# Kernel tuning notes

Measured on AMD Instinct MI355X. Metric: run time of the kernel, lower is better.

The kernel has to match this reference:

```python
import jax, jax.numpy as jnp
import numpy as np

E, C, H, W = 64, 8, 32, 32  # E zonotope rows (1 center + 63 error terms)


def setup_inputs() -> dict:
    key = jax.random.key(0)
    x = jax.random.normal(key, (E, C, H, W), dtype=jnp.float32)
    # Zero center => lower < 0 < upper everywhere, so every element crosses
    # and the number of new error terms equals C*H*W (fixed output shape).
    x = x.at[0].set(0.0)
    return {"x": x}


def reference(x):
    e = x.shape[0]
    content_shape = x.shape[1:]
    n = int(np.prod(content_shape))  # max possible new error terms

    err = jnp.sum(jnp.abs(x[1:]), axis=0)
    upper = x[0] + err
    lower = x[0] - err

    cross = (lower * upper < 0).astype(x.dtype)   # crossing-zero mask
    nonneg = (lower >= 0).astype(x.dtype)         # strictly positive mask

    lam = nonneg + cross * upper / (upper - lower)
    lam = jnp.where(jnp.isnan(lam), 0.5, lam)
    # torch assigns lambda via .data (detached from the autograd graph)
    lam = jax.lax.stop_gradient(lam)

    delta = jnp.maximum(-lam * lower, (1.0 - lam) * upper)

    head = (delta / 2 + lam * x[0]) * cross + x[0] * nonneg          # new center
    body = x[1:] * (lam * cross + nonneg)                            # scaled old error terms

    # Vectorized stream-compaction scatter replacing the scripted .item() loop:
    # element k (flat order) with cross==True goes to tail row cumsum(cross)[k]-1.
    flat_cond = cross.reshape(-1) > 0
    vals = (delta / 2).reshape(-1)
    rows = jnp.cumsum(flat_cond.astype(jnp.int32)) - 1
    rows = jnp.clip(rows, 0, n - 1)
    tail = jnp.zeros((n, n), dtype=x.dtype)
    # (row, col) pairs are unique per column; masked-out elements write 0 (no-op).
    tail = tail.at[rows, jnp.arange(n)].set(jnp.where(flat_cond, vals, 0.0))

    return jnp.concatenate(
        [head[None], body, tail.reshape((n,) + content_shape)], axis=0
    )
```

## Files before the change

### kernel.cpp

```cpp
#include <hip/hip_runtime.h>
#include <math.h>

#define EROWS 64
#define NCOL  8192
#define TAIL_OFF (EROWS * NCOL)
#define ROW_F4  (NCOL / 4)
#define BODY_F4 ((EROWS - 1) * ROW_F4)
#define BODY_BLOCKS (BODY_F4 / 256)
#define TAIL_BLOCKS NCOL

typedef float vf4 __attribute__((ext_vector_type(4)));
typedef int   vi4 __attribute__((ext_vector_type(4)));

#define WS_VAL(ws)     ((float*)(ws))
#define WS_FLAG(ws)    ((int*)((char*)(ws) + 32768))
#define WS_COLOF(ws)   ((int*)((char*)(ws) + 65536))
#define WS_TAILVAL(ws) ((float*)((char*)(ws) + 98304))
#define WS_COUNT(ws)   ((int*)((char*)(ws) + 131072))
#define WS_SCALE(ws)   ((float*)((char*)(ws) + 135168))

__global__ void colstats_kernel(const float* __restrict__ x,
                                float* __restrict__ out,
                                float* __restrict__ val,
                                int* __restrict__ flag,
                                float* __restrict__ scale) {
    int k = blockIdx.x * blockDim.x + threadIdx.x;
    if (k >= NCOL) return;

    float err = 0.f;
    for (int e = 1; e < EROWS; ++e)
        err += fabsf(x[e * NCOL + k]);

    float x0    = x[k];
    float upper = x0 + err;
    float lower = x0 - err;

    float cross  = (lower * upper < 0.f) ? 1.f : 0.f;
    float nonneg = (lower >= 0.f) ? 1.f : 0.f;

    float lam = nonneg + cross * upper / (upper - lower);
    if (isnan(lam)) lam = 0.5f;

    float delta = fmaxf(-lam * lower, (1.f - lam) * upper);

    out[k]   = (delta * 0.5f + lam * x0) * cross + x0 * nonneg;
    val[k]   = delta * 0.5f;
    flag[k]  = (cross > 0.f) ? 1 : 0;
    scale[k] = lam * cross + nonneg;
}

__global__ void scan_kernel(const float* __restrict__ val,
                            const int* __restrict__ flag,
                            int* __restrict__ colof,
                            float* __restrict__ tailval,
                            int* __restrict__ count) {
    const int t    = threadIdx.x;
    const int lane = t & 63;
    const int wave = t >> 6;
    const int PER  = NCOL / 256;

    int f[PER];
    int mysum = 0;
    const vi4* fp = (const vi4*)(flag + t * PER);
    for (int j = 0; j < PER / 4; ++j) {
        vi4 v = fp[j];
        f[4*j+0] = v.x; f[4*j+1] = v.y; f[4*j+2] = v.z; f[4*j+3] = v.w;
        mysum += v.x + v.y + v.z + v.w;
    }

    int s = mysum;
    for (int off = 1; off < 64; off <<= 1) {
        int v = __shfl_up(s, off);
        if (lane >= off) s += v;
    }

    __shared__ int wsum[4];
    if (lane == 63) wsum[wave] = s;
    __syncthreads();
    int wbase = 0;
    for (int w = 0; w < wave; ++w) wbase += wsum[w];

    int running = wbase + s - mysum;

    for (int j = 0; j < PER; ++j) {
        int k = t * PER + j;
        if (f[j]) {
            colof[running]   = k;
            tailval[running] = val[k];
            ++running;
        }
    }
    if (t == 255) *count = wsum[0] + wsum[1] + wsum[2] + wsum[3];
}

__global__ void write_kernel(const float* __restrict__ x,
                             const float* __restrict__ scale,
                             const int* __restrict__ colof,
                             const float* __restrict__ tailval,
                             const int* __restrict__ count,
                             float* __restrict__ out) {
    const int tid = threadIdx.x;

    if (blockIdx.x < BODY_BLOCKS) {
        int b = blockIdx.x * 256 + tid;
        int j = b & (ROW_F4 - 1);
        int e = 1 + (b >> 11);
        vf4 xv = ((const vf4*)x)[e * ROW_F4 + j];
        vf4 sv = ((const vf4*)scale)[j];
        ((vf4*)out)[e * ROW_F4 + j] = xv * sv;
    } else {
        int r   = blockIdx.x - BODY_BLOCKS;
        int cnt = *count;
        int   col = (r < cnt) ? colof[r]   : -1;
        float tv  = (r < cnt) ? tailval[r] : 0.f;

        vf4* rowp = (vf4*)out + (TAIL_OFF / 4) + (size_t)r * ROW_F4;
        #pragma unroll
        for (int i = 0; i < ROW_F4 / 256; ++i) {
            int j  = i * 256 + tid;
            int c0 = j << 2;
            vf4 v;
            v.x = (col == c0 + 0) ? tv : 0.f;
            v.y = (col == c0 + 1) ? tv : 0.f;
            v.z = (col == c0 + 2) ? tv : 0.f;
            v.w = (col == c0 + 3) ? tv : 0.f;
            __builtin_nontemporal_store(v, rowp + j);
        }
    }
}

extern "C" void kernel_launch(void* const* d_in, const int* in_sizes, int n_in,
                              void* d_out, int out_size, void* d_ws, size_t ws_size,
                              hipStream_t stream) {
    const float* x = (const float*)d_in[0];
    float* out = (float*)d_out;

    colstats_kernel<<<NCOL / 256, 256, 0, stream>>>(x, out, WS_VAL(d_ws),
                                                    WS_FLAG(d_ws), WS_SCALE(d_ws));
    scan_kernel<<<1, 256, 0, stream>>>(WS_VAL(d_ws), WS_FLAG(d_ws),
                                       WS_COLOF(d_ws), WS_TAILVAL(d_ws), WS_COUNT(d_ws));
    write_kernel<<<BODY_BLOCKS + TAIL_BLOCKS, 256, 0, stream>>>(
        x, WS_SCALE(d_ws), WS_COLOF(d_ws), WS_TAILVAL(d_ws), WS_COUNT(d_ws), out);
}
```

Baseline: 291.2 us.

## Fuse stats with body write and tail zero-fill; scatter diagonal afterwards

Merges column statistics, body scaling and the bulk zero-fill of the tail matrix into one kernel so the large fill does not wait for the scan. A small kernel then writes only the nonzero tail entries after the scan. This removes the per-element compare for the tail and the scale buffer round trip. The fill now uses regular stores instead of nontemporal stores, which may affect cache behaviour.

```diff
diff --git a/kernel.cpp b/kernel.cpp
--- a/kernel.cpp
+++ b/kernel.cpp
@@ -4,10 +4,11 @@
 #define EROWS 64
 #define NCOL  8192
 #define TAIL_OFF (EROWS * NCOL)
-#define ROW_F4  (NCOL / 4)
-#define BODY_F4 ((EROWS - 1) * ROW_F4)
-#define BODY_BLOCKS (BODY_F4 / 256)
-#define TAIL_BLOCKS NCOL
+#define TAIL_F4  (NCOL * NCOL / 4)
+
+#define STAT_BLOCKS 256
+#define FILL_F4_PER_BLOCK 4096
+#define FILL_BLOCKS (TAIL_F4 / FILL_F4_PER_BLOCK)
 
 typedef float vf4 __attribute__((ext_vector_type(4)));
 typedef int   vi4 __attribute__((ext_vector_type(4)));
@@ -17,36 +18,77 @@
 #define WS_COLOF(ws)   ((int*)((char*)(ws) + 65536))
 #define WS_TAILVAL(ws) ((float*)((char*)(ws) + 98304))
 #define WS_COUNT(ws)   ((int*)((char*)(ws) + 131072))
-#define WS_SCALE(ws)   ((float*)((char*)(ws) + 135168))
 
-__global__ void colstats_kernel(const float* __restrict__ x,
-                                float* __restrict__ out,
-                                float* __restrict__ val,
-                                int* __restrict__ flag,
-                                float* __restrict__ scale) {
-    int k = blockIdx.x * blockDim.x + threadIdx.x;
-    if (k >= NCOL) return;
+__global__ void fused_kernel(const float* __restrict__ x,
+                             float* __restrict__ out,
+                             float* __restrict__ val,
+                             int* __restrict__ flag) {
+    const int tid = threadIdx.x;
 
-    float err = 0.f;
-    for (int e = 1; e < EROWS; ++e)
-        err += fabsf(x[e * NCOL + k]);
+    if (blockIdx.x >= STAT_BLOCKS) {
+        vf4 z; z.x = 0.f; z.y = 0.f; z.z = 0.f; z.w = 0.f;
+        vf4* base = (vf4*)out + (TAIL_OFF / 4)
+                  + (size_t)(blockIdx.x - STAT_BLOCKS) * FILL_F4_PER_BLOCK;
+        #pragma unroll
+        for (int i = 0; i < 16; ++i)
+            base[i * 256 + tid] = z;
+        return;
+    }
 
-    float x0    = x[k];
-    float upper = x0 + err;
-    float lower = x0 - err;
+    __shared__ float part[256];
+    __shared__ float sc[32];
 
-    float cross  = (lower * upper < 0.f) ? 1.f : 0.f;
-    float nonneg = (lower >= 0.f) ? 1.f : 0.f;
+    const int c   = tid & 31;
+    const int eg  = tid >> 5;
+    const int col = blockIdx.x * 32 + c;
 
-    float lam = nonneg + cross * upper / (upper - lower);
-    if (isnan(lam)) lam = 0.5f;
+    float xv[8];
+    int   ev[8];
+    int   n = 0;
+    float s = 0.f;
+    #pragma unroll
+    for (int j = 0; j < 8; ++j) {
+        int e = eg + 8 * j;
+        if (e == 0) continue;
+        float v = x[e * NCOL + col];
+        xv[n] = v; ev[n] = e; ++n;
+        s += fabsf(v);
+    }
+    part[eg * 32 + c] = s;
+    __syncthreads();
 
-    float delta = fmaxf(-lam * lower, (1.f - lam) * upper);
+    if (tid < 32) {
+        float err = 0.f;
+        #pragma unroll
+        for (int g = 0; g < 8; ++g)
+            err += part[g * 32 + tid];
 
-    out[k]   = (delta * 0.5f + lam * x0) * cross + x0 * nonneg;
-    val[k]   = delta * 0.5f;
-    flag[k]  = (cross > 0.f) ? 1 : 0;
-    scale[k] = lam * cross + nonneg;
+        int   k  = blockIdx.x * 32 + tid;
+        float x0 = x[k];
+        float upper = x0 + err;
+        float lower = x0 - err;
+
+        float cross  = (lower * upper < 0.f) ? 1.f : 0.f;
+        float nonneg = (lower >= 0.f) ? 1.f : 0.f;
+
+        float lam = nonneg + cross * upper / (upper - lower);
+        if (isnan(lam)) lam = 0.5f;
+
+        float delta = fmaxf(-lam * lower, (1.f - lam) * upper);
+
+        out[k]   = (delta * 0.5f + lam * x0) * cross + x0 * nonneg;
+        val[k]   = delta * 0.5f;
+        flag[k]  = (cross > 0.f) ? 1 : 0;
+        sc[tid]  = lam * cross + nonneg;
+    }
+    __syncthreads();
+
+    float scl = sc[c];
+    #pragma unroll
+    for (int i = 0; i < 8; ++i) {
+        if (i < n)
+            out[ev[i] * NCOL + col] = xv[i] * scl;
+    }
 }
 
 __global__ void scan_kernel(const float* __restrict__ val,
@@ -93,40 +135,14 @@
     if (t == 255) *count = wsum[0] + wsum[1] + wsum[2] + wsum[3];
 }
 
-__global__ void write_kernel(const float* __restrict__ x,
-                             const float* __restrict__ scale,
-                             const int* __restrict__ colof,
-                             const float* __restrict__ tailval,
-                             const int* __restrict__ count,
-                             float* __restrict__ out) {
-    const int tid = threadIdx.x;
-
-    if (blockIdx.x < BODY_BLOCKS) {
-        int b = blockIdx.x * 256 + tid;
-        int j = b & (ROW_F4 - 1);
-        int e = 1 + (b >> 11);
-        vf4 xv = ((const vf4*)x)[e * ROW_F4 + j];
-        vf4 sv = ((const vf4*)scale)[j];
-        ((vf4*)out)[e * ROW_F4 + j] = xv * sv;
-    } else {
-        int r   = blockIdx.x - BODY_BLOCKS;
-        int cnt = *count;
-        int   col = (r < cnt) ? colof[r]   : -1;
-        float tv  = (r < cnt) ? tailval[r] : 0.f;
-
-        vf4* rowp = (vf4*)out + (TAIL_OFF / 4) + (size_t)r * ROW_F4;
-        #pragma unroll
-        for (int i = 0; i < ROW_F4 / 256; ++i) {
-            int j  = i * 256 + tid;
-            int c0 = j << 2;
-            vf4 v;
-            v.x = (col == c0 + 0) ? tv : 0.f;
-            v.y = (col == c0 + 1) ? tv : 0.f;
-            v.z = (col == c0 + 2) ? tv : 0.f;
-            v.w = (col == c0 + 3) ? tv : 0.f;
-            __builtin_nontemporal_store(v, rowp + j);
-        }
-    }
+__global__ void diag_kernel(const int* __restrict__ colof,
+                            const float* __restrict__ tailval,
+                            const int* __restrict__ count,
+                            float* __restrict__ out) {
+    int r = blockIdx.x * blockDim.x + threadIdx.x;
+    int cnt = *count;
+    if (r < cnt)
+        out[TAIL_OFF + (size_t)r * NCOL + colof[r]] = tailval[r];
 }
 
 extern "C" void kernel_launch(void* const* d_in, const int* in_sizes, int n_in,
@@ -135,10 +151,10 @@
     const float* x = (const float*)d_in[0];
     float* out = (float*)d_out;
 
-    colstats_kernel<<<NCOL / 256, 256, 0, stream>>>(x, out, WS_VAL(d_ws),
-                                                    WS_FLAG(d_ws), WS_SCALE(d_ws));
+    fused_kernel<<<STAT_BLOCKS + FILL_BLOCKS, 256, 0, stream>>>(
+        x, out, WS_VAL(d_ws), WS_FLAG(d_ws));
     scan_kernel<<<1, 256, 0, stream>>>(WS_VAL(d_ws), WS_FLAG(d_ws),
                                        WS_COLOF(d_ws), WS_TAILVAL(d_ws), WS_COUNT(d_ws));
-    write_kernel<<<BODY_BLOCKS + TAIL_BLOCKS, 256, 0, stream>>>(
-        x, WS_SCALE(d_ws), WS_COLOF(d_ws), WS_TAILVAL(d_ws), WS_COUNT(d_ws), out);
+    diag_kernel<<<NCOL / 256, 256, 0, stream>>>(WS_COLOF(d_ws), WS_TAILVAL(d_ws),
+                                                WS_COUNT(d_ws), out);
 }
```

Measured after the change: 278.0 us. 4.5% less time.
